# Performance work log

Measured on AMD Instinct MI355X. Metric: run time of the kernel, lower is better.

Reference implementation:

```python
import jax, jax.numpy as jnp
import numpy as np

# dims derived from init_kwargs
N_NODES = 100000            # type_mask.shape[0]
N0, N1 = 60000, 40000       # nodes per type
F0, F1 = 128, 64            # feats_dim_list
HID = 64                    # hidden_dim (= in_dim of layer1)
HEADS = 8
OUT = 16
ATTN_VEC = 128
E = 250000                  # metapath instances per metapath
L = 3                       # nodes per metapath instance (2 edge types)
NG = 8192                   # nodes in each minibatch DGL graph
B = 8192                    # number of target nodes
ETYPES = [[0, 1], [2, 3]]   # etypes_list; num_edge_type=4, RotatE0 -> 2 base relations


def setup_inputs() -> dict:
    ks = jax.random.split(jax.random.key(0), 20)
    g = lambda k, s, sc=1.0: sc * jax.random.normal(k, s, dtype=jnp.float32)
    return {
        "feat0": g(ks[0], (N0, F0)),
        "feat1": g(ks[1], (N1, F1)),
        "W0": g(ks[2], (HID, F0), 0.12),
        "b0": jnp.zeros((HID,), jnp.float32),
        "W1": g(ks[3], (HID, F1), 0.15),
        "b1": jnp.zeros((HID,), jnp.float32),
        "r_vec": g(ks[4], (2, HID // 2, 2), 0.2),
        "attn0": g(ks[5], (HEADS, HID), 0.2),
        "attn1": g(ks[6], (HEADS, HID), 0.2),
        "fc1_w": g(ks[7], (ATTN_VEC, HEADS * HID), 0.06),
        "fc1_b": jnp.zeros((ATTN_VEC,), jnp.float32),
        "fc2_w": g(ks[8], (1, ATTN_VEC), 0.1),
        "fc_w": g(ks[9], (OUT, HEADS * HID), 0.06),
        "fc_b": jnp.zeros((OUT,), jnp.float32),
        "idx0": jnp.arange(N0, dtype=jnp.int32),                 # type-0 node ids (contiguous block)
        "idx1": jnp.arange(N1, dtype=jnp.int32) + N0,            # type-1 node ids (offset block)
        "mp0_indices": jax.random.randint(ks[10], (E, L), 0, N_NODES, dtype=jnp.int32),
        "mp0_dst": jax.random.randint(ks[11], (E,), 0, NG, dtype=jnp.int32),
        "mp0_target": jax.random.randint(ks[12], (B,), 0, NG, dtype=jnp.int32),
        "mp1_indices": jax.random.randint(ks[13], (E, L), 0, N_NODES, dtype=jnp.int32),
        "mp1_dst": jax.random.randint(ks[14], (E,), 0, NG, dtype=jnp.int32),
        "mp1_target": jax.random.randint(ks[15], (B,), 0, NG, dtype=jnp.int32),
    }


def _cmul(a, b):
    # complex multiply on trailing dim of size 2
    re = a[..., 0] * b[..., 0] - a[..., 1] * b[..., 1]
    im = a[..., 0] * b[..., 1] + a[..., 1] * b[..., 0]
    return jnp.stack([re, im], axis=-1)


def reference(feat0, feat1, W0, b0, W1, b1, r_vec, attn0, attn1,
              fc1_w, fc1_b, fc2_w, fc_w, fc_b,
              idx0, idx1,
              mp0_indices, mp0_dst, mp0_target,
              mp1_indices, mp1_dst, mp1_target):
    # per-node-type linear scattered into a dense [N, HID] table (dropout=0 / eval)
    tf = jnp.zeros((N_NODES, HID), jnp.float32)
    tf = tf.at[idx0].set(feat0 @ W0.T + b0)
    tf = tf.at[idx1].set(feat1 @ W1.T + b1)

    # RotatE0: unit-modulus normalize, then double relations with conjugates
    rv = r_vec / jnp.linalg.norm(r_vec, axis=-1, keepdims=True)          # [2, HID//2, 2]
    conj = rv * jnp.array([1.0, -1.0], rv.dtype)
    rv_full = jnp.stack([rv, conj], axis=1).reshape(-1, HID // 2, 2)     # [4, HID//2, 2]

    def metapath(indices, dst, target, attn, etypes):
        edata = tf[indices].reshape(E, L, HID // 2, 2)   # gather metapath instances
        # suffix products of rotations: final[i] = prod_{j>=i} r[etypes[j]], final[L-1]=1
        final = [jnp.stack([jnp.ones(HID // 2, jnp.float32),
                            jnp.zeros(HID // 2, jnp.float32)], -1)]
        for i in range(L - 2, -1, -1):
            final.insert(0, _cmul(final[0], rv_full[etypes[i]]))
        finals = jnp.stack(final, axis=0)                # [L, HID//2, 2]
        edata = _cmul(edata, finals)                     # rotate every path position
        h = edata.reshape(E, L, HID).mean(axis=1)        # [E, HID] instance encoding
        # node-level attention (heads share h: torch tiles hidden across heads)
        a = jax.nn.leaky_relu(h @ attn.T, 0.01)          # [E, HEADS]
        m = jax.ops.segment_max(a, dst, num_segments=NG)
        ex = jnp.exp(a - m[dst])
        s = jax.ops.segment_sum(ex, dst, num_segments=NG)
        an = ex / s[dst]                                 # edge softmax per destination
        eft = jnp.einsum('eh,ed->ehd', an, h)            # [E, HEADS, HID]
        ft = jax.ops.segment_sum(eft, dst, num_segments=NG)
        ret = ft[target].reshape(B, HEADS * HID)
        return jax.nn.elu(ret)

    out0 = metapath(mp0_indices, mp0_dst, mp0_target, attn0, ETYPES[0])
    out1 = metapath(mp1_indices, mp1_dst, mp1_target, attn1, ETYPES[1])

    # metapath-level attention
    outs = jnp.stack([out0, out1], axis=0)               # [P, B, HEADS*HID]
    s1 = jnp.tanh(outs @ fc1_w.T + fc1_b)                # [P, B, ATTN_VEC]
    beta = jax.nn.softmax((s1.mean(axis=1) @ fc2_w.T)[:, 0], axis=0)  # [P]
    hagg = jnp.einsum('p,pbf->bf', beta, outs)           # [B, HEADS*HID]
    logits = hagg @ fc_w.T + fc_b                        # [B, OUT]
    return logits, hagg
```

## Files before the change

kernel.cpp:

```cpp
#include <hip/hip_runtime.h>
#include <hip/hip_fp16.h>
#include <math.h>

#define NNODES 100000
#define NT0 60000
#define NT1 40000
#define FD0 128
#define FD1 64
#define HID 64
#define HEADS 8
#define OUTD 16
#define AVEC 128
#define NE 250000
#define NG 8192
#define NB 8192

#define OFF_TF16    0ull
#define OFF_FINALS  3200000ull
#define OFF_A       3200512ull
#define OFF_ACC     3203584ull
#define OFF_BETA    3203840ull
#define OFF_P       3204096ull
#define OFF_SORTED  5604096ull
#define OFF_COUNTS  7604096ull
#define OFF_CURS    7620480ull
#define OFF_OFFS    7636864ull
#define OFF_FT      7653504ull

__global__ __launch_bounds__(256) void k_prep(const float* __restrict__ r_vec,
                       const float* __restrict__ attn0, const float* __restrict__ attn1,
                       float* __restrict__ finals, float* __restrict__ A,
                       float* __restrict__ acc, float* __restrict__ beta){
  __shared__ float2 fl[192];
  int t = threadIdx.x;
  if (t < 32){
    int j = t;
    const float2* rv = (const float2*)r_vec;
    float2 r0 = rv[j];
    float2 r1 = rv[32 + j];
    float n0 = rsqrtf(r0.x*r0.x + r0.y*r0.y);
    float n1 = rsqrtf(r1.x*r1.x + r1.y*r1.y);
    r0.x *= n0; r0.y *= n0; r1.x *= n1; r1.y *= n1;
    float2 rf1 = make_float2(r0.x, -r0.y);
    float2 rf3 = make_float2(r1.x, -r1.y);
    float2 F00 = make_float2(rf1.x*r0.x - rf1.y*r0.y, rf1.x*r0.y + rf1.y*r0.x);
    float2 F10 = make_float2(rf3.x*r1.x - rf3.y*r1.y, rf3.x*r1.y + rf3.y*r1.x);
    float2 one = make_float2(1.f, 0.f);
    float2* F = (float2*)finals;
    F[0*32+j] = F00; F[1*32+j] = rf1; F[2*32+j] = one;
    F[3*32+j] = F10; F[4*32+j] = rf3; F[5*32+j] = one;
    fl[0*32+j] = F00; fl[1*32+j] = rf1; fl[2*32+j] = one;
    fl[3*32+j] = F10; fl[4*32+j] = rf3; fl[5*32+j] = one;
  }
  __syncthreads();
  for (int idx = t; idx < 1536; idx += 256){
    int pair = idx & 31, k = (idx >> 5) & 7, pi = idx >> 8;
    const float* at = (pi >= 3) ? attn1 : attn0;
    float2 f = fl[pi*32 + pair];
    float a0 = at[k*64 + 2*pair], a1 = at[k*64 + 2*pair + 1];
    A[(pi*8+k)*64 + 2*pair]     = (f.x*a0 + f.y*a1) * (1.f/3.f);
    A[(pi*8+k)*64 + 2*pair + 1] = (f.x*a1 - f.y*a0) * (1.f/3.f);
  }
  acc[t] = 0.f;
  if (t < 2) beta[t] = 0.f;
}

__global__ __launch_bounds__(256) void k_transform2(const float* __restrict__ feat0,
                  const float* __restrict__ W0v, const float* __restrict__ b0v,
                  const int* __restrict__ idx0,
                  const float* __restrict__ feat1, const float* __restrict__ W1v,
                  const float* __restrict__ b1v, const int* __restrict__ idx1,
                  __half* __restrict__ tf16){
  __shared__ float Ax[32][68];
  __shared__ float Bs[32][68];
  const int nb0 = (NT0 + 63)/64;
  int bid = blockIdx.x;
  const float *feat, *W, *bias; const int* idx; int n_nodes, F, m0;
  if (bid < nb0){ feat=feat0; W=W0v; bias=b0v; idx=idx0; n_nodes=NT0; F=FD0; m0=bid*64; }
  else { feat=feat1; W=W1v; bias=b1v; idx=idx1; n_nodes=NT1; F=FD1; m0=(bid-nb0)*64; }
  int t = threadIdx.x;
  int tx = t & 15;
  int ty = t >> 4;
  int Fq = F >> 2;

  float acc[4][4];
  #pragma unroll
  for (int i = 0; i < 4; ++i)
    #pragma unroll
    for (int j = 0; j < 4; ++j) acc[i][j] = 0.f;

  const float4* feat4 = (const float4*)feat;
  const float4* W4 = (const float4*)W;

  for (int k0 = 0; k0 < F; k0 += 32){
    #pragma unroll
    for (int qq = 0; qq < 2; ++qq){
      int q = t + qq*256;
      int m = q >> 3, kq = q & 7;
      int gm = m0 + m; if (gm > n_nodes - 1) gm = n_nodes - 1;
      float4 v = feat4[(size_t)gm*Fq + (k0 >> 2) + kq];
      Ax[kq*4+0][m] = v.x; Ax[kq*4+1][m] = v.y; Ax[kq*4+2][m] = v.z; Ax[kq*4+3][m] = v.w;
    }
    #pragma unroll
    for (int qq = 0; qq < 2; ++qq){
      int q = t + qq*256;
      int d = q >> 3, kq = q & 7;
      float4 v = W4[(size_t)d*Fq + (k0 >> 2) + kq];
      Bs[kq*4+0][d] = v.x; Bs[kq*4+1][d] = v.y; Bs[kq*4+2][d] = v.z; Bs[kq*4+3][d] = v.w;
    }
    __syncthreads();
    #pragma unroll
    for (int kk = 0; kk < 32; ++kk){
      float4 a = *(const float4*)&Ax[kk][tx*4];
      float4 b = *(const float4*)&Bs[kk][ty*4];
      acc[0][0] += a.x*b.x; acc[0][1] += a.x*b.y; acc[0][2] += a.x*b.z; acc[0][3] += a.x*b.w;
      acc[1][0] += a.y*b.x; acc[1][1] += a.y*b.y; acc[1][2] += a.y*b.z; acc[1][3] += a.y*b.w;
      acc[2][0] += a.z*b.x; acc[2][1] += a.z*b.y; acc[2][2] += a.z*b.z; acc[2][3] += a.z*b.w;
      acc[3][0] += a.w*b.x; acc[3][1] += a.w*b.y; acc[3][2] += a.w*b.z; acc[3][3] += a.w*b.w;
    }
    __syncthreads();
  }

  float4 bv = *(const float4*)&bias[ty*4];
  #pragma unroll
  for (int i = 0; i < 4; ++i){
    int gm = m0 + tx*4 + i;
    if (gm < n_nodes){
      union { __half2 h2[2]; uint2 u; } pk;
      pk.h2[0] = __floats2half2_rn(acc[i][0] + bv.x, acc[i][1] + bv.y);
      pk.h2[1] = __floats2half2_rn(acc[i][2] + bv.z, acc[i][3] + bv.w);
      *(uint2*)&tf16[(size_t)idx[gm]*HID + ty*4] = pk.u;
    }
  }
}

__global__ __launch_bounds__(256) void k_pmat(const __half* __restrict__ tf16,
                                              const float* __restrict__ A,
                                              __half* __restrict__ P){
  __shared__ float tfl[64][65];
  __shared__ float Al[48][65];
  int t = threadIdx.x;
  int n0 = blockIdx.x * 64;
  for (int q = t; q < 3072; q += 256) Al[q >> 6][q & 63] = A[q];
  const __half2* tfh = (const __half2*)(tf16 + (size_t)n0*64);
  for (int q = t; q < 2048; q += 256){
    int n = q >> 5, dq = q & 31;
    float2 v = make_float2(0.f, 0.f);
    if (n0 + n < NNODES) v = __half22float2(tfh[n*32 + dq]);
    tfl[n][dq*2] = v.x; tfl[n][dq*2+1] = v.y;
  }
  __syncthreads();
  int nl = t >> 2, q = t & 3;
  float s[12];
  #pragma unroll
  for (int c = 0; c < 12; ++c) s[c] = 0.f;
  #pragma unroll 4
  for (int d = 0; d < 64; ++d){
    float tv = tfl[nl][d];
    #pragma unroll
    for (int c = 0; c < 12; ++c) s[c] += tv * Al[q*12 + c][d];
  }
  int gn = n0 + nl;
  if (gn < NNODES){
    #pragma unroll
    for (int c = 0; c < 12; ++c){
      int cg = q*12 + c;
      int p = cg >= 24;
      int w = cg - p*24;
      P[(size_t)p*2400000 + (size_t)gn*24 + w] = __float2half(s[c]);
    }
  }
}

__global__ void k_zeroi(int* __restrict__ p, int n){
  int t = blockIdx.x*blockDim.x + threadIdx.x;
  if (t < n) p[t] = 0;
}

__global__ void k_hist2(const int* __restrict__ d0, const int* __restrict__ d1,
                        int* __restrict__ counts){
  int e = blockIdx.x*blockDim.x + threadIdx.x;
  if (e < NE) atomicAdd(&counts[d0[e]], 1);
  else if (e < 2*NE) atomicAdd(&counts[NG + d1[e-NE]], 1);
}

__global__ __launch_bounds__(1024) void k_scan(const int* __restrict__ counts,
                                               int* __restrict__ offs,
                                               int* __restrict__ curs){
  __shared__ int lds[1024];
  int t = threadIdx.x;
  int base = t*16;
  int v[16]; int sum = 0;
  #pragma unroll
  for (int i = 0; i < 16; ++i){ v[i] = counts[base+i]; sum += v[i]; }
  lds[t] = sum;
  __syncthreads();
  for (int off = 1; off < 1024; off <<= 1){
    int x = (t >= off) ? lds[t-off] : 0;
    __syncthreads();
    lds[t] += x;
    __syncthreads();
  }
  int excl = lds[t] - sum;
  #pragma unroll
  for (int i = 0; i < 16; ++i){ offs[base+i] = excl; excl += v[i]; curs[base+i] = 0; }
  if (t == 1023) offs[2*NG] = excl;
}

__global__ void k_scatter2(const int* __restrict__ m0, const int* __restrict__ d0,
                           const int* __restrict__ m1, const int* __restrict__ d1,
                           const int* __restrict__ offs, int* __restrict__ curs,
                           int4* __restrict__ sorted){
  int e = blockIdx.x*blockDim.x + threadIdx.x;
  if (e >= 2*NE) return;
  const int* mp; int d;
  if (e < NE){ mp = m0 + (size_t)e*3; d = d0[e]; }
  else { mp = m1 + (size_t)(e-NE)*3; d = NG + d1[e-NE]; }
  int pos = offs[d] + atomicAdd(&curs[d], 1);
  sorted[pos] = make_int4(mp[0], mp[1], mp[2], 0);
}

__global__ __launch_bounds__(64) void k_seg(const __half* __restrict__ tf16,
                                            const __half* __restrict__ P,
                                            const int4* __restrict__ sorted,
                                            const int* __restrict__ offs,
                                            const float* __restrict__ finals,
                                            float* __restrict__ ft){
  int bid = blockIdx.x;
  int p = bid >> 13;
  int lane = threadIdx.x;
  int hw = lane >> 5, j = lane & 31;
  int start = offs[bid], end = offs[bid+1];
  float2* ftw = (float2*)(ft + (size_t)bid*512);
  if (start == end){
    #pragma unroll
    for (int kk = 0; kk < 4; ++kk) ftw[(hw*4+kk)*32 + j] = make_float2(0.f, 0.f);
    return;
  }
  const float2* F2 = (const float2*)(finals + p*192);
  float2 f0 = F2[j], f1 = F2[32 + j];
  const __half2* tfh = (const __half2*)tf16;
  const __half* Pp = P + (size_t)p*2400000;

  __shared__ int4 ndb[64];
  __shared__ float wb[64][8];

  float s[8], ur[8], ui[8];
  #pragma unroll
  for (int k = 0; k < 8; ++k){ s[k] = 0.f; ur[k] = 0.f; ui[k] = 0.f; }

  for (int c = start; c < end; c += 64){
    int n = end - c; if (n > 64) n = 64;
    if (lane < n){
      int4 nd = sorted[c + lane];
      ndb[lane] = nd;
      float4 rA = *(const float4*)(Pp + (size_t)nd.x*24);
      float4 rB = *(const float4*)(Pp + (size_t)nd.y*24 + 8);
      float4 rC = *(const float4*)(Pp + (size_t)nd.z*24 + 16);
      const __half2* ha = (const __half2*)&rA;
      const __half2* hb = (const __half2*)&rB;
      const __half2* hc = (const __half2*)&rC;
      float w[8];
      #pragma unroll
      for (int m = 0; m < 4; ++m){
        float2 va = __half22float2(ha[m]);
        float2 vb = __half22float2(hb[m]);
        float2 vc = __half22float2(hc[m]);
        float x0 = va.x + vb.x + vc.x;
        float x1 = va.y + vb.y + vc.y;
        x0 = x0 > 0.f ? x0 : 0.01f*x0;
        x1 = x1 > 0.f ? x1 : 0.01f*x1;
        w[2*m]   = __expf(x0);
        w[2*m+1] = __expf(x1);
      }
      *(float4*)&wb[lane][0] = make_float4(w[0], w[1], w[2], w[3]);
      *(float4*)&wb[lane][4] = make_float4(w[4], w[5], w[6], w[7]);
    }
    __syncthreads();
    int cend = c + n;
    for (int i = c + hw; i < cend; i += 2){
      int e = i - c;
      int4 nd = ndb[e];
      float4 wlo = *(const float4*)&wb[e][0];
      float4 whi = *(const float4*)&wb[e][4];
      float2 v0 = __half22float2(tfh[(size_t)nd.x*32 + j]);
      float2 v1 = __half22float2(tfh[(size_t)nd.y*32 + j]);
      float2 v2 = __half22float2(tfh[(size_t)nd.z*32 + j]);
      float hre = (v0.x*f0.x - v0.y*f0.y) + (v1.x*f1.x - v1.y*f1.y) + v2.x;
      float him = (v0.x*f0.y + v0.y*f0.x) + (v1.x*f1.y + v1.y*f1.x) + v2.y;
      ur[0] += wlo.x*hre; ui[0] += wlo.x*him; s[0] += wlo.x;
      ur[1] += wlo.y*hre; ui[1] += wlo.y*him; s[1] += wlo.y;
      ur[2] += wlo.z*hre; ui[2] += wlo.z*him; s[2] += wlo.z;
      ur[3] += wlo.w*hre; ui[3] += wlo.w*him; s[3] += wlo.w;
      ur[4] += whi.x*hre; ui[4] += whi.x*him; s[4] += whi.x;
      ur[5] += whi.y*hre; ui[5] += whi.y*him; s[5] += whi.y;
      ur[6] += whi.z*hre; ui[6] += whi.z*him; s[6] += whi.z;
      ur[7] += whi.w*hre; ui[7] += whi.w*him; s[7] += whi.w;
    }
    __syncthreads();
  }
  #pragma unroll
  for (int k = 0; k < 8; ++k){
    ur[k] += __shfl_xor(ur[k], 32);
    ui[k] += __shfl_xor(ui[k], 32);
    s[k]  += __shfl_xor(s[k], 32);
  }
  #pragma unroll
  for (int kk = 0; kk < 4; ++kk){
    int k = hw*4 + kk;
    float inv = 1.f / (3.f * s[k]);
    ftw[k*32 + j] = make_float2(ur[k]*inv, ui[k]*inv);
  }
}

__global__ __launch_bounds__(512) void k_s1g(const float* __restrict__ ft0,
                                             const float* __restrict__ ft1,
                                             const int* __restrict__ tgt0,
                                             const int* __restrict__ tgt1,
                                             const float* __restrict__ fc1_w,
                                             const float* __restrict__ fc1_b,
                                             float* __restrict__ acc_p){
  int bid = blockIdx.x;
  int bb = bid & 127;
  int p  = bid >> 7;
  const float* ft = p ? ft1 : ft0;
  const int* tgt  = p ? tgt1 : tgt0;

  __shared__ float Ax[32][68];
  __shared__ float Bs[32][132];
  __shared__ int   tl[64];
  __shared__ float red[128][17];

  int t = threadIdx.x;
  int tx = t & 15, ty = t >> 4;
  if (t < 64) tl[t] = tgt[bb*64 + t];
  __syncthreads();

  float acc[4][4];
  #pragma unroll
  for (int i = 0; i < 4; ++i)
    #pragma unroll
    for (int j = 0; j < 4; ++j) acc[i][j] = 0.f;

  const float4* W4 = (const float4*)fc1_w;

  for (int k0 = 0; k0 < 512; k0 += 32){
    {
      int m = t >> 3, kq = t & 7;
      const float4* row = (const float4*)(ft + (size_t)tl[m]*512);
      float4 v = row[(k0 >> 2) + kq];
      v.x = v.x > 0.f ? v.x : expm1f(v.x);
      v.y = v.y > 0.f ? v.y : expm1f(v.y);
      v.z = v.z > 0.f ? v.z : expm1f(v.z);
      v.w = v.w > 0.f ? v.w : expm1f(v.w);
      Ax[kq*4+0][m] = v.x; Ax[kq*4+1][m] = v.y; Ax[kq*4+2][m] = v.z; Ax[kq*4+3][m] = v.w;
    }
    #pragma unroll
    for (int qq = 0; qq < 2; ++qq){
      int q = t + qq*512;
      int d = q >> 3, kq = q & 7;
      float4 v = W4[(size_t)d*128 + (k0 >> 2) + kq];
      Bs[kq*4+0][d] = v.x; Bs[kq*4+1][d] = v.y; Bs[kq*4+2][d] = v.z; Bs[kq*4+3][d] = v.w;
    }
    __syncthreads();
    #pragma unroll
    for (int kk = 0; kk < 32; ++kk){
      float4 a = *(const float4*)&Ax[kk][tx*4];
      float4 b = *(const float4*)&Bs[kk][ty*4];
      acc[0][0] += a.x*b.x; acc[0][1] += a.x*b.y; acc[0][2] += a.x*b.z; acc[0][3] += a.x*b.w;
      acc[1][0] += a.y*b.x; acc[1][1] += a.y*b.y; acc[1][2] += a.y*b.z; acc[1][3] += a.y*b.w;
      acc[2][0] += a.z*b.x; acc[2][1] += a.z*b.y; acc[2][2] += a.z*b.z; acc[2][3] += a.z*b.w;
      acc[3][0] += a.w*b.x; acc[3][1] += a.w*b.y; acc[3][2] += a.w*b.z; acc[3][3] += a.w*b.w;
    }
    __syncthreads();
  }

  float4 bv = *(const float4*)&fc1_b[ty*4];
  float cs0 = 0.f, cs1 = 0.f, cs2 = 0.f, cs3 = 0.f;
  #pragma unroll
  for (int i = 0; i < 4; ++i){
    cs0 += tanhf(acc[i][0] + bv.x);
    cs1 += tanhf(acc[i][1] + bv.y);
    cs2 += tanhf(acc[i][2] + bv.z);
    cs3 += tanhf(acc[i][3] + bv.w);
  }
  red[ty*4+0][tx] = cs0;
  red[ty*4+1][tx] = cs1;
  red[ty*4+2][tx] = cs2;
  red[ty*4+3][tx] = cs3;
  __syncthreads();
  if (t < 128){
    float sv = 0.f;
    #pragma unroll
    for (int x = 0; x < 16; ++x) sv += red[t][x];
    atomicAdd(&acc_p[p*128 + t], sv);
  }
}

__global__ void k_beta(const float* __restrict__ acc, const float* __restrict__ fc2_w,
                       float* __restrict__ beta){
  int t = threadIdx.x;
  float s0 = acc[t]*fc2_w[t] + acc[t+64]*fc2_w[t+64];
  float s1 = acc[128+t]*fc2_w[t] + acc[192+t]*fc2_w[t+64];
  #pragma unroll
  for (int mask = 1; mask < 64; mask <<= 1){
    s0 += __shfl_xor(s0, mask, 64);
    s1 += __shfl_xor(s1, mask, 64);
  }
  if (t == 0){
    float z0 = s0 / (float)NB, z1 = s1 / (float)NB;
    float mz = fmaxf(z0, z1);
    float e0 = expf(z0 - mz), e1 = expf(z1 - mz);
    float inv = 1.f / (e0 + e1);
    beta[0] = e0*inv; beta[1] = e1*inv;
  }
}

__global__ void k_final(const float* __restrict__ ft0, const float* __restrict__ ft1,
                        const int* __restrict__ tgt0, const int* __restrict__ tgt1,
                        const float* __restrict__ beta, const float* __restrict__ fc_w,
                        const float* __restrict__ fc_b, float* __restrict__ d_out){
  __shared__ float lds[512];
  int b = blockIdx.x, t = threadIdx.x;
  float b0 = beta[0], b1 = beta[1];
  int g0 = tgt0[b], g1 = tgt1[b];
  float v0 = ft0[(size_t)g0*512 + t]; v0 = v0 > 0.f ? v0 : expm1f(v0);
  float v1 = ft1[(size_t)g1*512 + t]; v1 = v1 > 0.f ? v1 : expm1f(v1);
  float h = b0*v0 + b1*v1;
  lds[t] = h;
  d_out[(size_t)NB*OUTD + (size_t)b*512 + t] = h;
  __syncthreads();
  int o = t >> 5, j = t & 31;
  float s = 0.f;
  const float* w = fc_w + o*512;
  for (int d = j; d < 512; d += 32) s += lds[d]*w[d];
  #pragma unroll
  for (int mask = 1; mask < 32; mask <<= 1) s += __shfl_xor(s, mask, 32);
  if (j == 0) d_out[(size_t)b*OUTD + o] = s + fc_b[o];
}

extern "C" void kernel_launch(void* const* d_in, const int* in_sizes, int n_in,
                              void* d_out, int out_size, void* d_ws, size_t ws_size,
                              hipStream_t stream){
  const float* feat0  = (const float*)d_in[0];
  const float* feat1  = (const float*)d_in[1];
  const float* W0     = (const float*)d_in[2];
  const float* b0     = (const float*)d_in[3];
  const float* W1     = (const float*)d_in[4];
  const float* b1     = (const float*)d_in[5];
  const float* r_vec  = (const float*)d_in[6];
  const float* attn0  = (const float*)d_in[7];
  const float* attn1  = (const float*)d_in[8];
  const float* fc1_w  = (const float*)d_in[9];
  const float* fc1_b  = (const float*)d_in[10];
  const float* fc2_w  = (const float*)d_in[11];
  const float* fc_w   = (const float*)d_in[12];
  const float* fc_b   = (const float*)d_in[13];
  const int*   idx0   = (const int*)d_in[14];
  const int*   idx1   = (const int*)d_in[15];
  const int*   mpi0   = (const int*)d_in[16];
  const int*   mdst0  = (const int*)d_in[17];
  const int*   mtgt0  = (const int*)d_in[18];
  const int*   mpi1   = (const int*)d_in[19];
  const int*   mdst1  = (const int*)d_in[20];
  const int*   mtgt1  = (const int*)d_in[21];

  float* ws      = (float*)d_ws;
  __half* tf16   = (__half*)(ws + OFF_TF16);
  float* finals  = ws + OFF_FINALS;
  float* Amat    = ws + OFF_A;
  float* acc     = ws + OFF_ACC;
  float* beta    = ws + OFF_BETA;
  __half* P      = (__half*)(ws + OFF_P);
  int4*  sorted  = (int4*)(ws + OFF_SORTED);
  int*   counts  = (int*)(ws + OFF_COUNTS);
  int*   curs    = (int*)(ws + OFF_CURS);
  int*   offs    = (int*)(ws + OFF_OFFS);
  float* ft0     = ws + OFF_FT;
  float* ft1     = ws + OFF_FT + (size_t)NG*512;

  k_prep<<<1, 256, 0, stream>>>(r_vec, attn0, attn1, finals, Amat, acc, beta);
  k_zeroi<<<64, 256, 0, stream>>>(counts, 2*NG);
  k_hist2<<<(2*NE + 255)/256, 256, 0, stream>>>(mdst0, mdst1, counts);
  k_scan<<<1, 1024, 0, stream>>>(counts, offs, curs);
  k_scatter2<<<(2*NE + 255)/256, 256, 0, stream>>>(mpi0, mdst0, mpi1, mdst1,
                                                   offs, curs, sorted);

  k_transform2<<<(NT0 + 63)/64 + (NT1 + 63)/64, 256, 0, stream>>>(
      feat0, W0, b0, idx0, feat1, W1, b1, idx1, tf16);
  k_pmat<<<(NNODES + 63)/64, 256, 0, stream>>>(tf16, Amat, P);

  k_seg<<<2*NG, 64, 0, stream>>>(tf16, P, sorted, offs, finals, ws + OFF_FT);

  k_s1g<<<256, 512, 0, stream>>>(ft0, ft1, mtgt0, mtgt1, fc1_w, fc1_b, acc);
  k_beta<<<1, 64, 0, stream>>>(acc, fc2_w, beta);
  k_final<<<NB, 512, 0, stream>>>(ft0, ft1, mtgt0, mtgt1, beta, fc_w, fc_b,
                                  (float*)d_out);
}
```

Baseline: 262.6 us.

## Compute metapath attention over unique nodes weighted by target multiplicity counts

The metapath-level attention mean now runs over all NG graph nodes contiguously instead of gathering rows for each of the B targets. A histogram of target occurrences is built alongside the destination histogram, and each node's tanh row is weighted by its count. This removes the indirect row gather and lets the GEMM read ft rows contiguously. It keeps the same total work (8192 rows per metapath) while retiling the GEMM to 128-thread blocks with 32x128 tiles.

```diff
diff --git a/kernel.cpp b/kernel.cpp
--- a/kernel.cpp
+++ b/kernel.cpp
@@ -23,9 +23,10 @@
 #define OFF_P       3204096ull
 #define OFF_SORTED  5604096ull
 #define OFF_COUNTS  7604096ull
-#define OFF_CURS    7620480ull
-#define OFF_OFFS    7636864ull
-#define OFF_FT      7653504ull
+#define OFF_CNTT    7620480ull
+#define OFF_CURS    7636864ull
+#define OFF_OFFS    7653248ull
+#define OFF_FT      7669888ull
 
 __global__ __launch_bounds__(256) void k_prep(const float* __restrict__ r_vec,
                        const float* __restrict__ attn0, const float* __restrict__ attn1,
@@ -177,11 +178,14 @@
   if (t < n) p[t] = 0;
 }
 
-__global__ void k_hist2(const int* __restrict__ d0, const int* __restrict__ d1,
-                        int* __restrict__ counts){
+__global__ void k_hist3(const int* __restrict__ d0, const int* __restrict__ d1,
+                        const int* __restrict__ t0, const int* __restrict__ t1,
+                        int* __restrict__ counts, int* __restrict__ cntt){
   int e = blockIdx.x*blockDim.x + threadIdx.x;
   if (e < NE) atomicAdd(&counts[d0[e]], 1);
   else if (e < 2*NE) atomicAdd(&counts[NG + d1[e-NE]], 1);
+  else if (e < 2*NE + NB) atomicAdd(&cntt[t0[e-2*NE]], 1);
+  else if (e < 2*NE + 2*NB) atomicAdd(&cntt[NG + t1[e-2*NE-NB]], 1);
 }
 
 __global__ __launch_bounds__(1024) void k_scan(const int* __restrict__ counts,
@@ -313,86 +317,88 @@
   }
 }
 
-__global__ __launch_bounds__(512) void k_s1g(const float* __restrict__ ft0,
-                                             const float* __restrict__ ft1,
-                                             const int* __restrict__ tgt0,
-                                             const int* __restrict__ tgt1,
+__global__ __launch_bounds__(128) void k_s1g(const float* __restrict__ ftbase,
+                                             const int* __restrict__ cntt,
                                              const float* __restrict__ fc1_w,
                                              const float* __restrict__ fc1_b,
                                              float* __restrict__ acc_p){
+  __shared__ float An[32][34];
+  __shared__ float Bn[128][34];
+  __shared__ float red[128][5];
+
   int bid = blockIdx.x;
-  int bb = bid & 127;
-  int p  = bid >> 7;
-  const float* ft = p ? ft1 : ft0;
-  const int* tgt  = p ? tgt1 : tgt0;
-
-  __shared__ float Ax[32][68];
-  __shared__ float Bs[32][132];
-  __shared__ int   tl[64];
-  __shared__ float red[128][17];
-
+  int p  = bid >> 8;
+  int mb = bid & 255;
   int t = threadIdx.x;
-  int tx = t & 15, ty = t >> 4;
-  if (t < 64) tl[t] = tgt[bb*64 + t];
-  __syncthreads();
-
-  float acc[4][4];
-  #pragma unroll
-  for (int i = 0; i < 4; ++i)
+  int tx = t & 3;
+  int ty = t >> 2;
+
+  const float4* ft4 = (const float4*)(ftbase + ((size_t)p*NG + (size_t)mb*32)*512);
+  const float4* W4  = (const float4*)fc1_w;
+
+  float acc[8][4];
+  #pragma unroll
+  for (int i = 0; i < 8; ++i)
     #pragma unroll
     for (int j = 0; j < 4; ++j) acc[i][j] = 0.f;
 
-  const float4* W4 = (const float4*)fc1_w;
-
   for (int k0 = 0; k0 < 512; k0 += 32){
-    {
-      int m = t >> 3, kq = t & 7;
-      const float4* row = (const float4*)(ft + (size_t)tl[m]*512);
-      float4 v = row[(k0 >> 2) + kq];
+    #pragma unroll
+    for (int qq = 0; qq < 2; ++qq){
+      int q = t + qq*128;
+      int m = q >> 3, kq = q & 7;
+      float4 v = ft4[(size_t)m*128 + (k0 >> 2) + kq];
       v.x = v.x > 0.f ? v.x : expm1f(v.x);
       v.y = v.y > 0.f ? v.y : expm1f(v.y);
       v.z = v.z > 0.f ? v.z : expm1f(v.z);
       v.w = v.w > 0.f ? v.w : expm1f(v.w);
-      Ax[kq*4+0][m] = v.x; Ax[kq*4+1][m] = v.y; Ax[kq*4+2][m] = v.z; Ax[kq*4+3][m] = v.w;
-    }
-    #pragma unroll
-    for (int qq = 0; qq < 2; ++qq){
-      int q = t + qq*512;
+      *(float2*)&An[m][kq*4]     = make_float2(v.x, v.y);
+      *(float2*)&An[m][kq*4 + 2] = make_float2(v.z, v.w);
+    }
+    #pragma unroll
+    for (int qq = 0; qq < 8; ++qq){
+      int q = t + qq*128;
       int d = q >> 3, kq = q & 7;
       float4 v = W4[(size_t)d*128 + (k0 >> 2) + kq];
-      Bs[kq*4+0][d] = v.x; Bs[kq*4+1][d] = v.y; Bs[kq*4+2][d] = v.z; Bs[kq*4+3][d] = v.w;
-    }
-    __syncthreads();
-    #pragma unroll
-    for (int kk = 0; kk < 32; ++kk){
-      float4 a = *(const float4*)&Ax[kk][tx*4];
-      float4 b = *(const float4*)&Bs[kk][ty*4];
-      acc[0][0] += a.x*b.x; acc[0][1] += a.x*b.y; acc[0][2] += a.x*b.z; acc[0][3] += a.x*b.w;
-      acc[1][0] += a.y*b.x; acc[1][1] += a.y*b.y; acc[1][2] += a.y*b.z; acc[1][3] += a.y*b.w;
-      acc[2][0] += a.z*b.x; acc[2][1] += a.z*b.y; acc[2][2] += a.z*b.z; acc[2][3] += a.z*b.w;
-      acc[3][0] += a.w*b.x; acc[3][1] += a.w*b.y; acc[3][2] += a.w*b.z; acc[3][3] += a.w*b.w;
-    }
-    __syncthreads();
-  }
-
-  float4 bv = *(const float4*)&fc1_b[ty*4];
-  float cs0 = 0.f, cs1 = 0.f, cs2 = 0.f, cs3 = 0.f;
-  #pragma unroll
-  for (int i = 0; i < 4; ++i){
-    cs0 += tanhf(acc[i][0] + bv.x);
-    cs1 += tanhf(acc[i][1] + bv.y);
-    cs2 += tanhf(acc[i][2] + bv.z);
-    cs3 += tanhf(acc[i][3] + bv.w);
-  }
-  red[ty*4+0][tx] = cs0;
-  red[ty*4+1][tx] = cs1;
-  red[ty*4+2][tx] = cs2;
-  red[ty*4+3][tx] = cs3;
+      *(float2*)&Bn[d][kq*4]     = make_float2(v.x, v.y);
+      *(float2*)&Bn[d][kq*4 + 2] = make_float2(v.z, v.w);
+    }
+    __syncthreads();
+    #pragma unroll 4
+    for (int kk2 = 0; kk2 < 16; ++kk2){
+      float2 a2[8], b2[4];
+      #pragma unroll
+      for (int i = 0; i < 8; ++i) a2[i] = *(const float2*)&An[tx + 4*i][kk2*2];
+      #pragma unroll
+      for (int j = 0; j < 4; ++j) b2[j] = *(const float2*)&Bn[ty + 32*j][kk2*2];
+      #pragma unroll
+      for (int i = 0; i < 8; ++i)
+        #pragma unroll
+        for (int j = 0; j < 4; ++j)
+          acc[i][j] += a2[i].x*b2[j].x + a2[i].y*b2[j].y;
+    }
+    __syncthreads();
+  }
+
+  float cf[8];
+  #pragma unroll
+  for (int i = 0; i < 8; ++i)
+    cf[i] = (float)cntt[p*NG + mb*32 + tx + 4*i];
+  float csum[4];
+  #pragma unroll
+  for (int j = 0; j < 4; ++j){
+    float bv = fc1_b[ty + 32*j];
+    float sv = 0.f;
+    #pragma unroll
+    for (int i = 0; i < 8; ++i)
+      sv += cf[i] * tanhf(acc[i][j] + bv);
+    csum[j] = sv;
+  }
+  #pragma unroll
+  for (int j = 0; j < 4; ++j) red[ty + 32*j][tx] = csum[j];
   __syncthreads();
   if (t < 128){
-    float sv = 0.f;
-    #pragma unroll
-    for (int x = 0; x < 16; ++x) sv += red[t][x];
+    float sv = red[t][0] + red[t][1] + red[t][2] + red[t][3];
     atomicAdd(&acc_p[p*128 + t], sv);
   }
 }
@@ -474,14 +480,17 @@
   __half* P      = (__half*)(ws + OFF_P);
   int4*  sorted  = (int4*)(ws + OFF_SORTED);
   int*   counts  = (int*)(ws + OFF_COUNTS);
+  int*   cntt    = (int*)(ws + OFF_CNTT);
   int*   curs    = (int*)(ws + OFF_CURS);
   int*   offs    = (int*)(ws + OFF_OFFS);
-  float* ft0     = ws + OFF_FT;
-  float* ft1     = ws + OFF_FT + (size_t)NG*512;
+  float* ftb     = ws + OFF_FT;
+  float* ft0     = ftb;
+  float* ft1     = ftb + (size_t)NG*512;
 
   k_prep<<<1, 256, 0, stream>>>(r_vec, attn0, attn1, finals, Amat, acc, beta);
-  k_zeroi<<<64, 256, 0, stream>>>(counts, 2*NG);
-  k_hist2<<<(2*NE + 255)/256, 256, 0, stream>>>(mdst0, mdst1, counts);
+  k_zeroi<<<128, 256, 0, stream>>>(counts, 4*NG);
+  k_hist3<<<(2*NE + 2*NB + 255)/256, 256, 0, stream>>>(mdst0, mdst1, mtgt0, mtgt1,
+                                                       counts, cntt);
   k_scan<<<1, 1024, 0, stream>>>(counts, offs, curs);
   k_scatter2<<<(2*NE + 255)/256, 256, 0, stream>>>(mpi0, mdst0, mpi1, mdst1,
                                                    offs, curs, sorted);
@@ -490,9 +499,9 @@
       feat0, W0, b0, idx0, feat1, W1, b1, idx1, tf16);
   k_pmat<<<(NNODES + 63)/64, 256, 0, stream>>>(tf16, Amat, P);
 
-  k_seg<<<2*NG, 64, 0, stream>>>(tf16, P, sorted, offs, finals, ws + OFF_FT);
-
-  k_s1g<<<256, 512, 0, stream>>>(ft0, ft1, mtgt0, mtgt1, fc1_w, fc1_b, acc);
+  k_seg<<<2*NG, 64, 0, stream>>>(tf16, P, sorted, offs, finals, ftb);
+
+  k_s1g<<<512, 128, 0, stream>>>(ftb, cntt, fc1_w, fc1_b, acc);
   k_beta<<<1, 64, 0, stream>>>(acc, fc2_w, beta);
   k_final<<<NB, 512, 0, stream>>>(ft0, ft1, mtgt0, mtgt1, beta, fc_w, fc_b,
                                   (float*)d_out);
```

New measurement: 326.8 us. 24.4% more time.
